# Kernel tuning notes

Hardware: AMD Instinct MI355X
Metric: run time of the kernel (lower is better)

The kernel has to match this reference:

```python
import jax, jax.numpy as jnp
import numpy as np
from jax import lax

B, C, N = 4, 512, 4096
NH = 8
HD = C // NH          # 64
SR = 2                # sr_ratio
EPS = 1e-5            # BatchNorm eps (torch default)


def setup_inputs() -> dict:
    key = jax.random.key(0)
    ks = jax.random.split(key, 12)
    d = {}
    d["x"] = jax.random.normal(ks[0], (B, C, N), jnp.float32)
    d["y"] = jax.random.normal(ks[1], (B, C, N), jnp.float32)  # unused by forward (faithful to source)
    # Conv1d kernel-size-1 weights == (out_c, in_c) matrices; trunc_normal std=0.02 ~ normal*0.02
    d["Wq"] = jax.random.normal(ks[2], (C, C), jnp.float32) * 0.02
    d["Wk"] = jax.random.normal(ks[3], (C, C), jnp.float32) * 0.02
    # sr: Conv2d(dim, dim, kernel=SR, stride=SR), kaiming-ish init per _init_weights
    fan_out = SR * SR * C
    d["Wsr"] = jax.random.normal(ks[4], (C, C, SR, SR), jnp.float32) * np.sqrt(2.0 / fan_out)
    d["bsr"] = jnp.zeros((C,), jnp.float32)
    # BatchNorm1d(dim) in inference mode
    d["bn_gamma"] = 1.0 + 0.1 * jax.random.normal(ks[5], (C,), jnp.float32)
    d["bn_beta"] = 0.1 * jax.random.normal(ks[6], (C,), jnp.float32)
    d["bn_mean"] = 0.1 * jax.random.normal(ks[7], (C,), jnp.float32)
    d["bn_var"] = 1.0 + 0.1 * jnp.abs(jax.random.normal(ks[8], (C,), jnp.float32))
    d["Wproj"] = jax.random.normal(ks[9], (C, C), jnp.float32) * 0.02
    d["bproj"] = jnp.zeros((C,), jnp.float32)
    d["H"] = 64
    d["W"] = 64
    return d


def reference(x, y, Wq, Wk, Wsr, bsr, bn_gamma, bn_beta, bn_mean, bn_var, Wproj, bproj, H, W):
    scale = HD ** -0.5
    # q: Conv1d(k=1) -> (B,C,N) -> (B,NH,HD,N) -> (B,NH,N,HD)
    q = jnp.einsum('oc,bcn->bon', Wq, x).reshape(B, NH, HD, N).transpose(0, 1, 3, 2)
    # spatial reduction path (sr_ratio > 1): Conv2d stride SR, then BN (inference), then k-proj
    x4 = x.reshape(B, C, H, W)
    xsr = lax.conv_general_dilated(x4, Wsr, (SR, SR), 'VALID',
                                   dimension_numbers=('NCHW', 'OIHW', 'NCHW'))
    xsr = xsr + bsr[None, :, None, None]
    xsr = xsr.reshape(B, C, -1)  # (B, C, Nk), Nk = (H//SR)*(W//SR)
    inv_std = lax.rsqrt(bn_var + EPS)
    xsr = (xsr - bn_mean[None, :, None]) * (inv_std * bn_gamma)[None, :, None] + bn_beta[None, :, None]
    k = jnp.einsum('oc,bcn->bon', Wk, xsr).reshape(B, NH, HD, -1)  # (B,NH,HD,Nk)
    # v: mean over tokens, replicated per head -> effectively (B, C)
    v = jnp.mean(x, axis=2)  # (B, C)
    # scores + max over keys (no softmax)
    attn = jnp.einsum('bhnd,bhdk->bhnk', q, k) * scale  # (B,NH,N,Nk)
    attn = jnp.max(attn, axis=-1)                        # (B,NH,N)
    # out[b,c,n] = sum_h attn[b,h,n] * v[b,c]  (attn^T @ v, then transpose)
    out = jnp.sum(attn, axis=1)[:, None, :] * v[:, :, None]  # (B,C,N)
    out = jnp.einsum('oc,bcn->bon', Wproj, out) + bproj[None, :, None]
    return out
```

## Files before the change

### kernel.cpp

```cpp
#include <hip/hip_runtime.h>
#include <hip/hip_bf16.h>

constexpr int B_ = 4, C_ = 512, N_ = 4096, NH_ = 8, HD_ = 64;
constexpr int NK = 1024;
constexpr float SCALE = 0.125f;
constexpr float EPS = 1e-5f;

typedef __attribute__((ext_vector_type(8))) short bf16x8;
typedef __attribute__((ext_vector_type(4))) float f32x4;

__device__ __forceinline__ short bf16s(float f) {
    __hip_bfloat16 h = __float2bfloat16(f);
    return *reinterpret_cast<short*>(&h);
}
__device__ __forceinline__ float bf2f(short s) {
    return __bfloat162float(*reinterpret_cast<__hip_bfloat16*>(&s));
}

#define GLD16(gp, lp)                                                                     \
    __builtin_amdgcn_global_load_lds((const __attribute__((address_space(1))) void*)(gp), \
                                     (__attribute__((address_space(3))) void*)(lp), 16, 0, 0)

__global__ __launch_bounds__(256) void k_xw(const float* __restrict__ x,
                                            const float* __restrict__ Wq, const float* __restrict__ Wk,
// ... 45 lines not shown
            Wkp16[o * C_ + c] = bf16s(wk * sc);
            Wq16[o * C_ + c] = bf16s(Wq[o * C_ + c]);
            acc += wk * (sc * (bsr[c] - mean[c]) + beta[c]);
        }
        for (int m = 32; m; m >>= 1) acc += __shfl_xor(acc, m);
        if ((tid & 63) == 0) t[0][tid >> 6] = acc;
        __syncthreads();
        if (tid == 0) bk[o] = t[0][0] + t[0][1] + t[0][2] + t[0][3];
    } else {
        const int r = bid - 2560, kt = r & 31, ot = r >> 5;
        {
            const int cc = tid >> 2, q = tid & 3;
            const float* xr = Wsr + (size_t)(ot * 64 + cc) * 2048 + kt * 64;
#pragma unroll
            for (int jj = 0; jj < 4; ++jj) {
                float4 f = *reinterpret_cast<const float4*>(&xr[q * 16 + jj * 4]);
                int n = q * 16 + jj * 4;
                t[n + 0][cc] = f.x; t[n + 1][cc] = f.y;
                t[n + 2][cc] = f.z; t[n + 3][cc] = f.w;
            }
        }
        __syncthreads();
        {
            const int n = tid >> 2, c0 = (tid & 3) * 16;
            bf16x8 u0, u1;
#pragma unroll
            for (int j = 0; j < 8; ++j) {
                u0[j] = bf16s(t[n][c0 + j]);
                u1[j] = bf16s(t[n][c0 + 8 + j]);
            }
            int gkk = kt * 64 + n;
            int row2 = (gkk & 3) * 512 + (gkk >> 2);
            short* dst = WsrT + (size_t)row2 * C_ + ot * 64 + c0;
            *reinterpret_cast<bf16x8*>(dst) = u0;
            *reinterpret_cast<bf16x8*>(dst + 8) = u1;
        }
    }
}

template <int MT>
__device__ __forceinline__ void gemm_core(const short* __restrict__ Ag,
                                          const short* __restrict__ Bg, int K,
                                          short* Abuf, short* Bbuf,
                                          f32x4 (&acc)[MT][4]) {
    const int tid = threadIdx.x;
    const int w = tid >> 6, l = tid & 63;
    const int lr = l & 15, lg = l >> 4;
    const int wm = w >> 1, wn = w & 1;
    const int srow = tid >> 3, scol = (tid & 7) * 8;
    char* AbufC = (char*)Abuf;
    char* BbufC = (char*)Bbuf;
    for (int kt = 0; kt < K; kt += 64) {
#pragma unroll
        for (int i = 0; i < MT; ++i)
            GLD16(Ag + (size_t)(i * 32 + srow) * K + kt + scol, AbufC + i * 4096 + tid * 16);
#pragma unroll
        for (int i = 0; i < 4; ++i)
            GLD16(Bg + (size_t)(i * 32 + srow) * K + kt + scol, BbufC + i * 4096 + tid * 16);
        __syncthreads();
        bf16x8 af[MT][2], bfv[4][2];
#pragma unroll
        for (int mt = 0; mt < MT; ++mt)
#pragma unroll
            for (int ks = 0; ks < 2; ++ks)
                af[mt][ks] = *reinterpret_cast<const bf16x8*>(
                    &Abuf[(wm * MT * 16 + mt * 16 + lr) * 64 + ks * 32 + lg * 8]);
#pragma unroll
        for (int nt = 0; nt < 4; ++nt)
#pragma unroll
            for (int ks = 0; ks < 2; ++ks)
                bfv[nt][ks] = *reinterpret_cast<const bf16x8*>(
                    &Bbuf[(wn * 64 + nt * 16 + lr) * 64 + ks * 32 + lg * 8]);
#pragma unroll
        for (int mt = 0; mt < MT; ++mt)
#pragma unroll
            for (int nt = 0; nt < 4; ++nt) {
                acc[mt][nt] = __builtin_amdgcn_mfma_f32_16x16x32_bf16(af[mt][0], bfv[nt][0], acc[mt][nt], 0, 0, 0);
                acc[mt][nt] = __builtin_amdgcn_mfma_f32_16x16x32_bf16(af[mt][1], bfv[nt][1], acc[mt][nt], 0, 0, 0);
            }
        __syncthreads();
    }
}

__global__ __launch_bounds__(256) void k_wck64(const short* __restrict__ WsrT,
                                               const short* __restrict__ Wkp16,
                                               short* __restrict__ Wck16) {
    __shared__ short Ab[64 * 64];
    __shared__ short Bb[64 * 64];
    const int m0 = blockIdx.x * 64;
    const int n0 = blockIdx.y * 64;
    const int tid = threadIdx.x, w = tid >> 6, l = tid & 63;
    const int lr = l & 15, lg = l >> 4, wm = w >> 1, wn = w & 1;
    const int srow = tid >> 3, scol = (tid & 7) * 8;
    f32x4 acc[2][2];
#pragma unroll
    for (int i = 0; i < 2; ++i)
#pragma unroll
        for (int j = 0; j < 2; ++j) acc[i][j] = (f32x4){0.f, 0.f, 0.f, 0.f};
    char* AbC = (char*)Ab;
    char* BbC = (char*)Bb;
    for (int kt = 0; kt < 512; kt += 64) {
#pragma unroll
        for (int j = 0; j < 2; ++j) {
            GLD16(WsrT + (size_t)(m0 + j * 32 + srow) * 512 + kt + scol, AbC + j * 4096 + tid * 16);
            GLD16(Wkp16 + (size_t)(n0 + j * 32 + srow) * 512 + kt + scol, BbC + j * 4096 + tid * 16);
        }
        __syncthreads();
        bf16x8 af[2][2], bfv[2][2];
#pragma unroll
        for (int mt = 0; mt < 2; ++mt)
#pragma unroll
            for (int ks = 0; ks < 2; ++ks)
                af[mt][ks] = *reinterpret_cast<const bf16x8*>(
                    &Ab[(wm * 32 + mt * 16 + lr) * 64 + ks * 32 + lg * 8]);
#pragma unroll
        for (int nt = 0; nt < 2; ++nt)
#pragma unroll
            for (int ks = 0; ks < 2; ++ks)
                bfv[nt][ks] = *reinterpret_cast<const bf16x8*>(
                    &Bb[(wn * 32 + nt * 16 + lr) * 64 + ks * 32 + lg * 8]);
#pragma unroll
        for (int mt = 0; mt < 2; ++mt)
#pragma unroll
            for (int nt = 0; nt < 2; ++nt) {
                acc[mt][nt] = __builtin_amdgcn_mfma_f32_16x16x32_bf16(af[mt][0], bfv[nt][0], acc[mt][nt], 0, 0, 0);
                acc[mt][nt] = __builtin_amdgcn_mfma_f32_16x16x32_bf16(af[mt][1], bfv[nt][1], acc[mt][nt], 0, 0, 0);
            }
        __syncthreads();
    }
#pragma unroll
    for (int mt = 0; mt < 2; ++mt)
#pragma unroll
        for (int nt = 0; nt < 2; ++nt) {
            int kk0 = m0 + wm * 32 + mt * 16 + lg * 4;
            int o = n0 + wn * 32 + nt * 16 + lr;
            short4 u;
            u.x = bf16s(acc[mt][nt][0]);
            u.y = bf16s(acc[mt][nt][1]);
            u.z = bf16s(acc[mt][nt][2]);
            u.w = bf16s(acc[mt][nt][3]);
            *reinterpret_cast<short4*>(&Wck16[(size_t)o * 2048 + kk0]) = u;
        }
}

__global__ __launch_bounds__(256) void k_gemm_qk2(const short* __restrict__ xT,
                                                  const short* __restrict__ Wq16,
                                                  const short* __restrict__ Wck16,
                                                  short* __restrict__ kp,
                                                  short* __restrict__ q2) {
    __shared__ short Abuf[128 * 64];
    __shared__ short Bbuf[128 * 64];
    f32x4 acc[4][4];
#pragma unroll
    for (int i = 0; i < 4; ++i)
#pragma unroll
        for (int j = 0; j < 4; ++j) acc[i][j] = (f32x4){0.f, 0.f, 0.f, 0.f};
    const int bid = blockIdx.x;
    const int tid = threadIdx.x, l = tid & 63, w = tid >> 6;
    const int lr = l & 15, lg = l >> 4, wm = w >> 1, wn = w & 1;
    const int srow = tid >> 3, scol = (tid & 7) * 8;
    char* AbufC = (char*)Abuf;
    char* BbufC = (char*)Bbuf;

    if (bid < 512) {
        const int s = bid >> 7;
        const int dy = s >> 1, dx = s & 1;
        const int r2 = bid & 127;
        const int n0 = (r2 >> 2) * 128;
        const int m0 = (r2 & 3) * 128;
        for (int kt2 = 0; kt2 < 512; kt2 += 64) {
#pragma unroll
            for (int i = 0; i < 4; ++i) {
                int bp = n0 + i * 32 + srow;
                int b = bp >> 10, p = bp & 1023;
                int n = ((p >> 5) * 2 + dy) * 64 + (p & 31) * 2 + dx;
                GLD16(xT + ((size_t)(b * N_ + n)) * C_ + kt2 + scol, AbufC + i * 4096 + tid * 16);
            }
#pragma unroll
            for (int i = 0; i < 4; ++i)
                GLD16(Wck16 + (size_t)(m0 + i * 32 + srow) * 2048 + s * 512 + kt2 + scol,
                      BbufC + i * 4096 + tid * 16);
            __syncthreads();
            bf16x8 af[4][2], bfv[4][2];
#pragma unroll
            for (int mt = 0; mt < 4; ++mt)
#pragma unroll
                for (int ks = 0; ks < 2; ++ks)
                    af[mt][ks] = *reinterpret_cast<const bf16x8*>(
                        &Abuf[(wm * 64 + mt * 16 + lr) * 64 + ks * 32 + lg * 8]);
#pragma unroll
            for (int nt = 0; nt < 4; ++nt)
#pragma unroll
                for (int ks = 0; ks < 2; ++ks)
                    bfv[nt][ks] = *reinterpret_cast<const bf16x8*>(
                        &Bbuf[(wn * 64 + nt * 16 + lr) * 64 + ks * 32 + lg * 8]);
#pragma unroll
            for (int mt = 0; mt < 4; ++mt)
#pragma unroll
                for (int nt = 0; nt < 4; ++nt) {
                    acc[mt][nt] = __builtin_amdgcn_mfma_f32_16x16x32_bf16(af[mt][0], bfv[nt][0], acc[mt][nt], 0, 0, 0);
                    acc[mt][nt] = __builtin_amdgcn_mfma_f32_16x16x32_bf16(af[mt][1], bfv[nt][1], acc[mt][nt], 0, 0, 0);
                }
            __syncthreads();
        }
        short* kps = kp + (size_t)s * (4096 * 512);
#pragma unroll
        for (int mt = 0; mt < 4; ++mt)
#pragma unroll
            for (int nt = 0; nt < 4; ++nt) {
                int o = m0 + wn * 64 + nt * 16 + lr;
#pragma unroll
                for (int r = 0; r < 4; ++r) {
                    int bp = n0 + wm * 64 + mt * 16 + lg * 4 + r;
                    kps[(size_t)bp * 512 + o] = bf16s(acc[mt][nt][r]);
                }
            }
    } else {
        const int bq = bid - 512;
        const int m0 = (bq & 3) * 128, n0 = (bq >> 2) * 128;
        gemm_core<4>(Wq16 + (size_t)m0 * 512, xT + (size_t)n0 * 512, 512, Abuf, Bbuf, acc);
#pragma unroll
        for (int mt = 0; mt < 4; ++mt) {
            const int o0 = m0 + wm * 64 + mt * 16 + lg * 4;
            const int h = o0 >> 6, d0 = o0 & 63;
#pragma unroll
            for (int nt = 0; nt < 4; ++nt) {
                int ng = n0 + wn * 64 + nt * 16 + lr;
                int b = ng >> 12, n = ng & 4095;
                short4 u;
                u.x = bf16s(acc[mt][nt][0]);
                u.y = bf16s(acc[mt][nt][1]);
                u.z = bf16s(acc[mt][nt][2]);
                u.w = bf16s(acc[mt][nt][3]);
                *reinterpret_cast<short4*>(&q2[(((size_t)(b * NH_ + h)) * N_ + n) * HD_ + d0]) = u;
            }
        }
    }
}

__global__ __launch_bounds__(256) void k_kredpv(const short* __restrict__ kp,
                                                const float* __restrict__ bk,
                                                const float* __restrict__ vpart,
                                                const float* __restrict__ Wproj,
                                                short* __restrict__ k3,
                                                float* __restrict__ pv) {
    const int bid = blockIdx.x, tid = threadIdx.x;
    if (bid < 4096) {
        const int bp = bid, b = bp >> 10, p = bp & 1023;
        const int o = tid * 2;
        const short* k0 = kp + (size_t)bp * 512 + o;
        float2 bb = *reinterpret_cast<const float2*>(&bk[o]);
        float sx = bb.x, sy = bb.y;
#pragma unroll
        for (int s = 0; s < 4; ++s) {
            short2 v2 = *reinterpret_cast<const short2*>(k0 + (size_t)s * (4096 * 512));
            sx += bf2f(v2.x);
            sy += bf2f(v2.y);
        }
        short2 u;
        u.x = bf16s(sx);
        u.y = bf16s(sy);
        const int h = o >> 6, d = o & 63;
        *reinterpret_cast<short2*>(&k3[(((size_t)(b * NH_ + h)) * NK + p) * HD_ + d]) = u;
    } else {
        const int r = bid - 4096, oc = r & 7, b = r >> 3;
        __shared__ float vs[512];
        float2 s = {0.f, 0.f};
        for (int y = 0; y < 64; ++y) {
            float2 f = *reinterpret_cast<const float2*>(&vpart[((size_t)(y * B_ + b)) * C_ + tid * 2]);
            s.x += f.x; s.y += f.y;
        }
        vs[tid * 2] = s.x * (1.f / N_);
        vs[tid * 2 + 1] = s.y * (1.f / N_);
        __syncthreads();
        const int w = tid >> 6, l = tid & 63;
#pragma unroll 4
        for (int i = 0; i < 16; ++i) {
            int o = oc * 64 + i * 4 + w;
            const float* wr = Wproj + (size_t)o * C_;
            float4 a = *reinterpret_cast<const float4*>(&wr[l * 8]);
            float4 b4 = *reinterpret_cast<const float4*>(&wr[l * 8 + 4]);
            float acc = a.x * vs[l * 8] + a.y * vs[l * 8 + 1] + a.z * vs[l * 8 + 2] + a.w * vs[l * 8 + 3] +
                        b4.x * vs[l * 8 + 4] + b4.y * vs[l * 8 + 5] + b4.z * vs[l * 8 + 6] + b4.w * vs[l * 8 + 7];
            for (int m = 32; m; m >>= 1) acc += __shfl_xor(acc, m);
            if (l == 0) pv[b * C_ + o] = acc;
        }
    }
}

__global__ __launch_bounds__(256) void k_attn3(const short* __restrict__ k3,
                                               const short* __restrict__ q2,
                                               float* __restrict__ am) {
    const int b = blockIdx.z, h = blockIdx.y, n0 = blockIdx.x * 256;
    const int w = threadIdx.x >> 6, l = threadIdx.x & 63;
    const int lr = l & 15, lg = l >> 4;
    const short* qb = q2 + ((size_t)(b * NH_ + h)) * N_ * HD_;
    const short* kb = k3 + ((size_t)(b * NH_ + h)) * NK * HD_;

    bf16x8 bq[16][2];
#pragma unroll
    for (int nt = 0; nt < 16; ++nt)
#pragma unroll
        for (int ks = 0; ks < 2; ++ks)
            bq[nt][ks] = *reinterpret_cast<const bf16x8*>(
                &qb[(size_t)(n0 + nt * 16 + lr) * HD_ + ks * 32 + lg * 8]);

    float rmax[16];
#pragma unroll
    for (int nt = 0; nt < 16; ++nt) rmax[nt] = -3.4e38f;

    const short* kw = kb + (size_t)(w * 256) * HD_;
    const short* s0 = kw + (size_t)lr * HD_ + lg * 8;
    bf16x8 a0 = *reinterpret_cast<const bf16x8*>(s0);
    bf16x8 a1 = *reinterpret_cast<const bf16x8*>(s0 + 32);
    for (int t = 0; t < 16; ++t) {
        bf16x8 c0 = a0, c1 = a1;
        if (t < 15) {
            const short* s2 = kw + (size_t)((t + 1) * 16 + lr) * HD_ + lg * 8;
            a0 = *reinterpret_cast<const bf16x8*>(s2);
            a1 = *reinterpret_cast<const bf16x8*>(s2 + 32);
        }
        __builtin_amdgcn_s_setprio(1);
#pragma unroll
        for (int nt = 0; nt < 16; ++nt) {
            f32x4 acc = {0.f, 0.f, 0.f, 0.f};
            acc = __builtin_amdgcn_mfma_f32_16x16x32_bf16(c0, bq[nt][0], acc, 0, 0, 0);
            acc = __builtin_amdgcn_mfma_f32_16x16x32_bf16(c1, bq[nt][1], acc, 0, 0, 0);
            rmax[nt] = fmaxf(fmaxf(fmaxf(fmaxf(acc[0], acc[1]), acc[2]), acc[3]), rmax[nt]);
        }
        __builtin_amdgcn_s_setprio(0);
    }
#pragma unroll
    for (int nt = 0; nt < 16; ++nt) {
        float m = rmax[nt];
        m = fmaxf(m, __shfl_xor(m, 16));
        m = fmaxf(m, __shfl_xor(m, 32));
        rmax[nt] = m;
    }
    __shared__ float sm[4][256];
    if (lg == 0) {
#pragma unroll
        for (int nt = 0; nt < 16; ++nt) sm[w][nt * 16 + lr] = rmax[nt];
    }
    __syncthreads();
    {
        const int tid = threadIdx.x;
        float m = fmaxf(fmaxf(sm[0][tid], sm[1][tid]),
                        fmaxf(sm[2][tid], sm[3][tid]));
        am[((size_t)(b * NH_ + h)) * N_ + n0 + tid] = SCALE * m;
    }
}

__global__ __launch_bounds__(256) void k_final(const float* __restrict__ pv, const float* __restrict__ am,
                                               const float* __restrict__ bproj, float* __restrict__ out) {
    const int b = blockIdx.z, o0 = blockIdx.y * 64 + (threadIdx.x >> 5) * 8;
    const int n = blockIdx.x * 128 + (threadIdx.x & 31) * 4;
    float4 s = {0.f, 0.f, 0.f, 0.f};
#pragma unroll
    for (int h = 0; h < NH_; ++h) {
        float4 a = *reinterpret_cast<const float4*>(&am[((size_t)(b * NH_ + h)) * N_ + n]);
        s.x += a.x; s.y += a.y; s.z += a.z; s.w += a.w;
    }
    float* ob = out + (size_t)b * C_ * N_ + n;
    const float* pvb = pv + b * C_;
#pragma unroll
    for (int i = 0; i < 8; ++i) {
        int o = o0 + i;
        float p = pvb[o], bp = bproj[o];
        float4 r = {p * s.x + bp, p * s.y + bp, p * s.z + bp, p * s.w + bp};
        *reinterpret_cast<float4*>(&ob[(size_t)o * N_]) = r;
    }
}

extern "C" void kernel_launch(void* const* d_in, const int* in_sizes, int n_in,
                              void* d_out, int out_size, void* d_ws, size_t ws_size,
                              hipStream_t stream) {
    const float* x     = (const float*)d_in[0];
    const float* Wq    = (const float*)d_in[2];
    const float* Wk    = (const float*)d_in[3];
    const float* Wsr   = (const float*)d_in[4];
    const float* bsr   = (const float*)d_in[5];
    const float* gamma = (const float*)d_in[6];
    const float* beta  = (const float*)d_in[7];
    const float* mean  = (const float*)d_in[8];
    const float* var   = (const float*)d_in[9];
    const float* Wproj = (const float*)d_in[10];
    const float* bproj = (const float*)d_in[11];
    float* out = (float*)d_out;

    char* ws = (char*)d_ws;
    float* vpart = (float*)(ws + 0);
    float* pv    = (float*)(ws + 524288);
    float* bk    = (float*)(ws + 532480);
    float* am    = (float*)(ws + 536576);
    short* Wq16  = (short*)(ws + 1060864);
    short* Wkp16 = (short*)(ws + 1585152);
    short* WsrT  = (short*)(ws + 2109440);
    short* Wck16 = (short*)(ws + 4206592);
    short* xT    = (short*)(ws + 6303744);
    short* q2    = (short*)(ws + 23080960);
    short* k3    = (short*)(ws + 39858176);
    short* kp    = (short*)(ws + 44052480);

    k_xw<<<dim3(2816), 256, 0, stream>>>(x, Wq, Wk, gamma, beta, mean, var, bsr, Wsr,
                                         xT, vpart, Wq16, Wkp16, bk, WsrT);
    k_wck64<<<dim3(32, 8), 256, 0, stream>>>(WsrT, Wkp16, Wck16);
    k_gemm_qk2<<<dim3(1024), 256, 0, stream>>>(xT, Wq16, Wck16, kp, q2);
    k_kredpv<<<dim3(4128), 256, 0, stream>>>(kp, bk, vpart, Wproj, k3, pv);
    k_attn3<<<dim3(16, NH_, B_), 256, 0, stream>>>(k3, q2, am);
    k_final<<<dim3(32, 8, B_), 256, 0, stream>>>(pv, am, bproj, out);
}
```

Baseline: 101.8 us.

## Fuse attention max with output projection and merge pv into weight-combine kernel

```diff
diff --git a/kernel.cpp b/kernel.cpp
--- a/kernel.cpp
+++ b/kernel.cpp
@@ -151,188 +151,72 @@
     }
 }
 
-__global__ __launch_bounds__(256) void k_wck64(const short* __restrict__ WsrT,
+__global__ __launch_bounds__(256) void k_wckpv(const short* __restrict__ WsrT,
                                                const short* __restrict__ Wkp16,
-                                               short* __restrict__ Wck16) {
-    __shared__ short Ab[64 * 64];
-    __shared__ short Bb[64 * 64];
-    const int m0 = blockIdx.x * 64;
-    const int n0 = blockIdx.y * 64;
-    const int tid = threadIdx.x, w = tid >> 6, l = tid & 63;
-    const int lr = l & 15, lg = l >> 4, wm = w >> 1, wn = w & 1;
-    const int srow = tid >> 3, scol = (tid & 7) * 8;
-    f32x4 acc[2][2];
-#pragma unroll
-    for (int i = 0; i < 2; ++i)
-#pragma unroll
-        for (int j = 0; j < 2; ++j) acc[i][j] = (f32x4){0.f, 0.f, 0.f, 0.f};
-    char* AbC = (char*)Ab;
-    char* BbC = (char*)Bb;
-    for (int kt = 0; kt < 512; kt += 64) {
-#pragma unroll
-        for (int j = 0; j < 2; ++j) {
-            GLD16(WsrT + (size_t)(m0 + j * 32 + srow) * 512 + kt + scol, AbC + j * 4096 + tid * 16);
-            GLD16(Wkp16 + (size_t)(n0 + j * 32 + srow) * 512 + kt + scol, BbC + j * 4096 + tid * 16);
-        }
-        __syncthreads();
-        bf16x8 af[2][2], bfv[2][2];
-#pragma unroll
-        for (int mt = 0; mt < 2; ++mt)
-#pragma unroll
-            for (int ks = 0; ks < 2; ++ks)
-                af[mt][ks] = *reinterpret_cast<const bf16x8*>(
-                    &Ab[(wm * 32 + mt * 16 + lr) * 64 + ks * 32 + lg * 8]);
-#pragma unroll
-        for (int nt = 0; nt < 2; ++nt)
-#pragma unroll
-            for (int ks = 0; ks < 2; ++ks)
-                bfv[nt][ks] = *reinterpret_cast<const bf16x8*>(
-                    &Bb[(wn * 32 + nt * 16 + lr) * 64 + ks * 32 + lg * 8]);
-#pragma unroll
-        for (int mt = 0; mt < 2; ++mt)
-#pragma unroll
-            for (int nt = 0; nt < 2; ++nt) {
-                acc[mt][nt] = __builtin_amdgcn_mfma_f32_16x16x32_bf16(af[mt][0], bfv[nt][0], acc[mt][nt], 0, 0, 0);
-                acc[mt][nt] = __builtin_amdgcn_mfma_f32_16x16x32_bf16(af[mt][1], bfv[nt][1], acc[mt][nt], 0, 0, 0);
-            }
-        __syncthreads();
-    }
-#pragma unroll
-    for (int mt = 0; mt < 2; ++mt)
-#pragma unroll
-        for (int nt = 0; nt < 2; ++nt) {
-            int kk0 = m0 + wm * 32 + mt * 16 + lg * 4;
-            int o = n0 + wn * 32 + nt * 16 + lr;
-            short4 u;
-            u.x = bf16s(acc[mt][nt][0]);
-            u.y = bf16s(acc[mt][nt][1]);
-            u.z = bf16s(acc[mt][nt][2]);
-            u.w = bf16s(acc[mt][nt][3]);
-            *reinterpret_cast<short4*>(&Wck16[(size_t)o * 2048 + kk0]) = u;
-        }
-}
-
-__global__ __launch_bounds__(256) void k_gemm_qk2(const short* __restrict__ xT,
-                                                  const short* __restrict__ Wq16,
-                                                  const short* __restrict__ Wck16,
-                                                  short* __restrict__ kp,
-                                                  short* __restrict__ q2) {
-    __shared__ short Abuf[128 * 64];
-    __shared__ short Bbuf[128 * 64];
-    f32x4 acc[4][4];
-#pragma unroll
-    for (int i = 0; i < 4; ++i)
-#pragma unroll
-        for (int j = 0; j < 4; ++j) acc[i][j] = (f32x4){0.f, 0.f, 0.f, 0.f};
-    const int bid = blockIdx.x;
-    const int tid = threadIdx.x, l = tid & 63, w = tid >> 6;
-    const int lr = l & 15, lg = l >> 4, wm = w >> 1, wn = w & 1;
-    const int srow = tid >> 3, scol = (tid & 7) * 8;
-    char* AbufC = (char*)Abuf;
-    char* BbufC = (char*)Bbuf;
-
-    if (bid < 512) {
-        const int s = bid >> 7;
-        const int dy = s >> 1, dx = s & 1;
-        const int r2 = bid & 127;
-        const int n0 = (r2 >> 2) * 128;
-        const int m0 = (r2 & 3) * 128;
-        for (int kt2 = 0; kt2 < 512; kt2 += 64) {
-#pragma unroll
-            for (int i = 0; i < 4; ++i) {
-                int bp = n0 + i * 32 + srow;
-                int b = bp >> 10, p = bp & 1023;
-                int n = ((p >> 5) * 2 + dy) * 64 + (p & 31) * 2 + dx;
-                GLD16(xT + ((size_t)(b * N_ + n)) * C_ + kt2 + scol, AbufC + i * 4096 + tid * 16);
-            }
-#pragma unroll
-            for (int i = 0; i < 4; ++i)
-                GLD16(Wck16 + (size_t)(m0 + i * 32 + srow) * 2048 + s * 512 + kt2 + scol,
-                      BbufC + i * 4096 + tid * 16);
+                                               const float* __restrict__ vpart,
+                                               const float* __restrict__ Wproj,
+                                               short* __restrict__ Wck16,
+                                               float* __restrict__ pv) {
+    const int bid = blockIdx.x, tid = threadIdx.x;
+    if (bid < 256) {
+        __shared__ short Ab[64 * 64];
+        __shared__ short Bb[64 * 64];
+        const int m0 = (bid & 31) * 64;
+        const int n0 = (bid >> 5) * 64;
+        const int w = tid >> 6, l = tid & 63;
+        const int lr = l & 15, lg = l >> 4, wm = w >> 1, wn = w & 1;
+        const int srow = tid >> 3, scol = (tid & 7) * 8;
+        f32x4 acc[2][2];
+#pragma unroll
+        for (int i = 0; i < 2; ++i)
+#pragma unroll
+            for (int j = 0; j < 2; ++j) acc[i][j] = (f32x4){0.f, 0.f, 0.f, 0.f};
+        char* AbC = (char*)Ab;
+        char* BbC = (char*)Bb;
+        for (int kt = 0; kt < 512; kt += 64) {
+#pragma unroll
+            for (int j = 0; j < 2; ++j) {
+                GLD16(WsrT + (size_t)(m0 + j * 32 + srow) * 512 + kt + scol, AbC + j * 4096 + tid * 16);
+                GLD16(Wkp16 + (size_t)(n0 + j * 32 + srow) * 512 + kt + scol, BbC + j * 4096 + tid * 16);
+            }
             __syncthreads();
-            bf16x8 af[4][2], bfv[4][2];
-#pragma unroll
-            for (int mt = 0; mt < 4; ++mt)
+            bf16x8 af[2][2], bfv[2][2];
+#pragma unroll
+            for (int mt = 0; mt < 2; ++mt)
 #pragma unroll
                 for (int ks = 0; ks < 2; ++ks)
                     af[mt][ks] = *reinterpret_cast<const bf16x8*>(
-                        &Abuf[(wm * 64 + mt * 16 + lr) * 64 + ks * 32 + lg * 8]);
-#pragma unroll
-            for (int nt = 0; nt < 4; ++nt)
+                        &Ab[(wm * 32 + mt * 16 + lr) * 64 + ks * 32 + lg * 8]);
+#pragma unroll
+            for (int nt = 0; nt < 2; ++nt)
 #pragma unroll
                 for (int ks = 0; ks < 2; ++ks)
                     bfv[nt][ks] = *reinterpret_cast<const bf16x8*>(
-                        &Bbuf[(wn * 64 + nt * 16 + lr) * 64 + ks * 32 + lg * 8]);
-#pragma unroll
-            for (int mt = 0; mt < 4; ++mt)
-#pragma unroll
-                for (int nt = 0; nt < 4; ++nt) {
+                        &Bb[(wn * 32 + nt * 16 + lr) * 64 + ks * 32 + lg * 8]);
+#pragma unroll
+            for (int mt = 0; mt < 2; ++mt)
+#pragma unroll
+                for (int nt = 0; nt < 2; ++nt) {
                     acc[mt][nt] = __builtin_amdgcn_mfma_f32_16x16x32_bf16(af[mt][0], bfv[nt][0], acc[mt][nt], 0, 0, 0);
                     acc[mt][nt] = __builtin_amdgcn_mfma_f32_16x16x32_bf16(af[mt][1], bfv[nt][1], acc[mt][nt], 0, 0, 0);
                 }
             __syncthreads();
         }
-        short* kps = kp + (size_t)s * (4096 * 512);
-#pragma unroll
-        for (int mt = 0; mt < 4; ++mt)
-#pragma unroll
-            for (int nt = 0; nt < 4; ++nt) {
-                int o = m0 + wn * 64 + nt * 16 + lr;
-#pragma unroll
-                for (int r = 0; r < 4; ++r) {
-                    int bp = n0 + wm * 64 + mt * 16 + lg * 4 + r;
-                    kps[(size_t)bp * 512 + o] = bf16s(acc[mt][nt][r]);
-                }
-            }
-    } else {
-        const int bq = bid - 512;
-        const int m0 = (bq & 3) * 128, n0 = (bq >> 2) * 128;
-        gemm_core<4>(Wq16 + (size_t)m0 * 512, xT + (size_t)n0 * 512, 512, Abuf, Bbuf, acc);
-#pragma unroll
-        for (int mt = 0; mt < 4; ++mt) {
-            const int o0 = m0 + wm * 64 + mt * 16 + lg * 4;
-            const int h = o0 >> 6, d0 = o0 & 63;
-#pragma unroll
-            for (int nt = 0; nt < 4; ++nt) {
-                int ng = n0 + wn * 64 + nt * 16 + lr;
-                int b = ng >> 12, n = ng & 4095;
+#pragma unroll
+        for (int mt = 0; mt < 2; ++mt)
+#pragma unroll
+            for (int nt = 0; nt < 2; ++nt) {
+                int kk0 = m0 + wm * 32 + mt * 16 + lg * 4;
+                int o = n0 + wn * 32 + nt * 16 + lr;
                 short4 u;
                 u.x = bf16s(acc[mt][nt][0]);
                 u.y = bf16s(acc[mt][nt][1]);
                 u.z = bf16s(acc[mt][nt][2]);
                 u.w = bf16s(acc[mt][nt][3]);
-                *reinterpret_cast<short4*>(&q2[(((size_t)(b * NH_ + h)) * N_ + n) * HD_ + d0]) = u;
-            }
-        }
-    }
-}
-
-__global__ __launch_bounds__(256) void k_kredpv(const short* __restrict__ kp,
-                                                const float* __restrict__ bk,
-                                                const float* __restrict__ vpart,
-                                                const float* __restrict__ Wproj,
-                                                short* __restrict__ k3,
-                                                float* __restrict__ pv) {
-    const int bid = blockIdx.x, tid = threadIdx.x;
-    if (bid < 4096) {
-        const int bp = bid, b = bp >> 10, p = bp & 1023;
-        const int o = tid * 2;
-        const short* k0 = kp + (size_t)bp * 512 + o;
-        float2 bb = *reinterpret_cast<const float2*>(&bk[o]);
-        float sx = bb.x, sy = bb.y;
-#pragma unroll
-        for (int s = 0; s < 4; ++s) {
-            short2 v2 = *reinterpret_cast<const short2*>(k0 + (size_t)s * (4096 * 512));
-            sx += bf2f(v2.x);
-            sy += bf2f(v2.y);
-        }
-        short2 u;
-        u.x = bf16s(sx);
-        u.y = bf16s(sy);
-        const int h = o >> 6, d = o & 63;
-        *reinterpret_cast<short2*>(&k3[(((size_t)(b * NH_ + h)) * NK + p) * HD_ + d]) = u;
+                *reinterpret_cast<short4*>(&Wck16[(size_t)o * 2048 + kk0]) = u;
+            }
     } else {
-        const int r = bid - 4096, oc = r & 7, b = r >> 3;
+        const int r = bid - 256, oc = r & 7, b = r >> 3;
         __shared__ float vs[512];
         float2 s = {0.f, 0.f};
         for (int y = 0; y < 64; ++y) {
@@ -357,87 +241,201 @@
     }
 }
 
-__global__ __launch_bounds__(256) void k_attn3(const short* __restrict__ k3,
+__global__ __launch_bounds__(256) void k_gemm_qk2(const short* __restrict__ xT,
+                                                  const short* __restrict__ Wq16,
+                                                  const short* __restrict__ Wck16,
+                                                  short* __restrict__ kp,
+                                                  short* __restrict__ q2) {
+    __shared__ short Abuf[128 * 64];
+    __shared__ short Bbuf[128 * 64];
+    f32x4 acc[4][4];
+#pragma unroll
+    for (int i = 0; i < 4; ++i)
+#pragma unroll
+        for (int j = 0; j < 4; ++j) acc[i][j] = (f32x4){0.f, 0.f, 0.f, 0.f};
+    const int bid = (blockIdx.x & 7) * 128 + (blockIdx.x >> 3);
+    const int tid = threadIdx.x, l = tid & 63, w = tid >> 6;
+    const int lr = l & 15, lg = l >> 4, wm = w >> 1, wn = w & 1;
+    const int srow = tid >> 3, scol = (tid & 7) * 8;
+    char* AbufC = (char*)Abuf;
+    char* BbufC = (char*)Bbuf;
+
+    if (bid < 512) {
+        const int s = bid >> 7;
+        const int dy = s >> 1, dx = s & 1;
+        const int r2 = bid & 127;
+        const int n0 = (r2 >> 2) * 128;
+        const int m0 = (r2 & 3) * 128;
+        for (int kt2 = 0; kt2 < 512; kt2 += 64) {
+#pragma unroll
+            for (int i = 0; i < 4; ++i) {
+                int bp = n0 + i * 32 + srow;
+                int b = bp >> 10, p = bp & 1023;
+                int n = ((p >> 5) * 2 + dy) * 64 + (p & 31) * 2 + dx;
+                GLD16(xT + ((size_t)(b * N_ + n)) * C_ + kt2 + scol, AbufC + i * 4096 + tid * 16);
+            }
+#pragma unroll
+            for (int i = 0; i < 4; ++i)
+                GLD16(Wck16 + (size_t)(m0 + i * 32 + srow) * 2048 + s * 512 + kt2 + scol,
+                      BbufC + i * 4096 + tid * 16);
+            __syncthreads();
+            bf16x8 af[4][2], bfv[4][2];
+#pragma unroll
+            for (int mt = 0; mt < 4; ++mt)
+#pragma unroll
+                for (int ks = 0; ks < 2; ++ks)
+                    af[mt][ks] = *reinterpret_cast<const bf16x8*>(
+                        &Abuf[(wm * 64 + mt * 16 + lr) * 64 + ks * 32 + lg * 8]);
+#pragma unroll
+            for (int nt = 0; nt < 4; ++nt)
+#pragma unroll
+                for (int ks = 0; ks < 2; ++ks)
+                    bfv[nt][ks] = *reinterpret_cast<const bf16x8*>(
+                        &Bbuf[(wn * 64 + nt * 16 + lr) * 64 + ks * 32 + lg * 8]);
+#pragma unroll
+            for (int mt = 0; mt < 4; ++mt)
+#pragma unroll
+                for (int nt = 0; nt < 4; ++nt) {
+                    acc[mt][nt] = __builtin_amdgcn_mfma_f32_16x16x32_bf16(af[mt][0], bfv[nt][0], acc[mt][nt], 0, 0, 0);
+                    acc[mt][nt] = __builtin_amdgcn_mfma_f32_16x16x32_bf16(af[mt][1], bfv[nt][1], acc[mt][nt], 0, 0, 0);
+                }
+            __syncthreads();
+        }
+        short* kps = kp + (size_t)s * (4096 * 512);
+#pragma unroll
+        for (int mt = 0; mt < 4; ++mt)
+#pragma unroll
+            for (int nt = 0; nt < 4; ++nt) {
+                int o = m0 + wn * 64 + nt * 16 + lr;
+#pragma unroll
+                for (int r = 0; r < 4; ++r) {
+                    int bp = n0 + wm * 64 + mt * 16 + lg * 4 + r;
+                    kps[(size_t)bp * 512 + o] = bf16s(acc[mt][nt][r]);
+                }
+            }
+    } else {
+        const int bq = bid - 512;
+        const int m0 = (bq & 3) * 128, n0 = (bq >> 2) * 128;
+        gemm_core<4>(Wq16 + (size_t)m0 * 512, xT + (size_t)n0 * 512, 512, Abuf, Bbuf, acc);
+#pragma unroll
+        for (int mt = 0; mt < 4; ++mt) {
+            const int o0 = m0 + wm * 64 + mt * 16 + lg * 4;
+            const int h = o0 >> 6, d0 = o0 & 63;
+#pragma unroll
+            for (int nt = 0; nt < 4; ++nt) {
+                int ng = n0 + wn * 64 + nt * 16 + lr;
+                int b = ng >> 12, n = ng & 4095;
+                short4 u;
+                u.x = bf16s(acc[mt][nt][0]);
+                u.y = bf16s(acc[mt][nt][1]);
+                u.z = bf16s(acc[mt][nt][2]);
+                u.w = bf16s(acc[mt][nt][3]);
+                *reinterpret_cast<short4*>(&q2[(((size_t)(b * NH_ + h)) * N_ + n) * HD_ + d0]) = u;
+            }
+        }
+    }
+}
+
+__global__ __launch_bounds__(256) void k_kred(const short* __restrict__ kp,
+                                              const float* __restrict__ bk,
+                                              short* __restrict__ k3) {
+    const int r = blockIdx.x * 4 + (threadIdx.x >> 6);
+    const int o0 = (threadIdx.x & 63) * 8;
+    const int b = r >> 10, p = r & 1023;
+    const short* base = kp + (size_t)r * 512 + o0;
+    float s[8];
+    float4 b0 = *reinterpret_cast<const float4*>(&bk[o0]);
+    float4 b1 = *reinterpret_cast<const float4*>(&bk[o0 + 4]);
+    s[0] = b0.x; s[1] = b0.y; s[2] = b0.z; s[3] = b0.w;
+    s[4] = b1.x; s[5] = b1.y; s[6] = b1.z; s[7] = b1.w;
+#pragma unroll
+    for (int sp = 0; sp < 4; ++sp) {
+        bf16x8 v = *reinterpret_cast<const bf16x8*>(base + (size_t)sp * (4096 * 512));
+#pragma unroll
+        for (int j = 0; j < 8; ++j) s[j] += bf2f(v[j]);
+    }
+    bf16x8 u;
+#pragma unroll
+    for (int j = 0; j < 8; ++j) u[j] = bf16s(s[j]);
+    const int h = o0 >> 6, d = o0 & 63;
+    *reinterpret_cast<bf16x8*>(&k3[(((size_t)(b * NH_ + h)) * NK + p) * HD_ + d]) = u;
+}
+
+__global__ __launch_bounds__(512) void k_attnf(const short* __restrict__ k3,
                                                const short* __restrict__ q2,
-                                               float* __restrict__ am) {
-    const int b = blockIdx.z, h = blockIdx.y, n0 = blockIdx.x * 256;
-    const int w = threadIdx.x >> 6, l = threadIdx.x & 63;
+                                               const float* __restrict__ pv,
+                                               const float* __restrict__ bproj,
+                                               float* __restrict__ out) {
+    const int b = blockIdx.y, n0 = blockIdx.x * 64;
+    const int tid = threadIdx.x, w = tid >> 6, l = tid & 63;
     const int lr = l & 15, lg = l >> 4;
-    const short* qb = q2 + ((size_t)(b * NH_ + h)) * N_ * HD_;
-    const short* kb = k3 + ((size_t)(b * NH_ + h)) * NK * HD_;
-
-    bf16x8 bq[16][2];
-#pragma unroll
-    for (int nt = 0; nt < 16; ++nt)
-#pragma unroll
-        for (int ks = 0; ks < 2; ++ks)
-            bq[nt][ks] = *reinterpret_cast<const bf16x8*>(
-                &qb[(size_t)(n0 + nt * 16 + lr) * HD_ + ks * 32 + lg * 8]);
-
-    float rmax[16];
-#pragma unroll
-    for (int nt = 0; nt < 16; ++nt) rmax[nt] = -3.4e38f;
-
-    const short* kw = kb + (size_t)(w * 256) * HD_;
-    const short* s0 = kw + (size_t)lr * HD_ + lg * 8;
-    bf16x8 a0 = *reinterpret_cast<const bf16x8*>(s0);
-    bf16x8 a1 = *reinterpret_cast<const bf16x8*>(s0 + 32);
-    for (int t = 0; t < 16; ++t) {
-        bf16x8 c0 = a0, c1 = a1;
-        if (t < 15) {
-            const short* s2 = kw + (size_t)((t + 1) * 16 + lr) * HD_ + lg * 8;
-            a0 = *reinterpret_cast<const bf16x8*>(s2);
-            a1 = *reinterpret_cast<const bf16x8*>(s2 + 32);
-        }
-        __builtin_amdgcn_s_setprio(1);
-#pragma unroll
-        for (int nt = 0; nt < 16; ++nt) {
-            f32x4 acc = {0.f, 0.f, 0.f, 0.f};
-            acc = __builtin_amdgcn_mfma_f32_16x16x32_bf16(c0, bq[nt][0], acc, 0, 0, 0);
-            acc = __builtin_amdgcn_mfma_f32_16x16x32_bf16(c1, bq[nt][1], acc, 0, 0, 0);
-            rmax[nt] = fmaxf(fmaxf(fmaxf(fmaxf(acc[0], acc[1]), acc[2]), acc[3]), rmax[nt]);
-        }
-        __builtin_amdgcn_s_setprio(0);
-    }
-#pragma unroll
-    for (int nt = 0; nt < 16; ++nt) {
-        float m = rmax[nt];
-        m = fmaxf(m, __shfl_xor(m, 16));
-        m = fmaxf(m, __shfl_xor(m, 32));
-        rmax[nt] = m;
-    }
-    __shared__ float sm[4][256];
-    if (lg == 0) {
-#pragma unroll
-        for (int nt = 0; nt < 16; ++nt) sm[w][nt * 16 + lr] = rmax[nt];
-    }
-    __syncthreads();
-    {
-        const int tid = threadIdx.x;
-        float m = fmaxf(fmaxf(sm[0][tid], sm[1][tid]),
-                        fmaxf(sm[2][tid], sm[3][tid]));
-        am[((size_t)(b * NH_ + h)) * N_ + n0 + tid] = SCALE * m;
-    }
-}
-
-__global__ __launch_bounds__(256) void k_final(const float* __restrict__ pv, const float* __restrict__ am,
-                                               const float* __restrict__ bproj, float* __restrict__ out) {
-    const int b = blockIdx.z, o0 = blockIdx.y * 64 + (threadIdx.x >> 5) * 8;
-    const int n = blockIdx.x * 128 + (threadIdx.x & 31) * 4;
-    float4 s = {0.f, 0.f, 0.f, 0.f};
-#pragma unroll
+    __shared__ float sm[8][64];
+    __shared__ float ssum[64];
+    if (tid < 64) ssum[tid] = 0.f;
+
     for (int h = 0; h < NH_; ++h) {
-        float4 a = *reinterpret_cast<const float4*>(&am[((size_t)(b * NH_ + h)) * N_ + n]);
-        s.x += a.x; s.y += a.y; s.z += a.z; s.w += a.w;
-    }
-    float* ob = out + (size_t)b * C_ * N_ + n;
+        const short* qb = q2 + ((size_t)(b * NH_ + h)) * N_ * HD_;
+        const short* kb = k3 + ((size_t)(b * NH_ + h)) * NK * HD_ + (size_t)(w * 128) * HD_;
+        bf16x8 bq[4][2];
+#pragma unroll
+        for (int nt = 0; nt < 4; ++nt)
+#pragma unroll
+            for (int ks = 0; ks < 2; ++ks)
+                bq[nt][ks] = *reinterpret_cast<const bf16x8*>(
+                    &qb[(size_t)(n0 + nt * 16 + lr) * HD_ + ks * 32 + lg * 8]);
+        float rmax[4];
+#pragma unroll
+        for (int nt = 0; nt < 4; ++nt) rmax[nt] = -3.4e38f;
+
+        const short* s0p = kb + (size_t)lr * HD_ + lg * 8;
+        bf16x8 a0 = *reinterpret_cast<const bf16x8*>(s0p);
+        bf16x8 a1 = *reinterpret_cast<const bf16x8*>(s0p + 32);
+        for (int t = 0; t < 8; ++t) {
+            bf16x8 c0 = a0, c1 = a1;
+            if (t < 7) {
+                const short* s2 = kb + (size_t)((t + 1) * 16 + lr) * HD_ + lg * 8;
+                a0 = *reinterpret_cast<const bf16x8*>(s2);
+                a1 = *reinterpret_cast<const bf16x8*>(s2 + 32);
+            }
+            __builtin_amdgcn_s_setprio(1);
+#pragma unroll
+            for (int nt = 0; nt < 4; ++nt) {
+                f32x4 acc = {0.f, 0.f, 0.f, 0.f};
+                acc = __builtin_amdgcn_mfma_f32_16x16x32_bf16(c0, bq[nt][0], acc, 0, 0, 0);
+                acc = __builtin_amdgcn_mfma_f32_16x16x32_bf16(c1, bq[nt][1], acc, 0, 0, 0);
+                rmax[nt] = fmaxf(fmaxf(fmaxf(fmaxf(acc[0], acc[1]), acc[2]), acc[3]), rmax[nt]);
+            }
+            __builtin_amdgcn_s_setprio(0);
+        }
+#pragma unroll
+        for (int nt = 0; nt < 4; ++nt) {
+            float m = rmax[nt];
+            m = fmaxf(m, __shfl_xor(m, 16));
+            m = fmaxf(m, __shfl_xor(m, 32));
+            rmax[nt] = m;
+        }
+        if (lg == 0) {
+#pragma unroll
+            for (int nt = 0; nt < 4; ++nt) sm[w][nt * 16 + lr] = rmax[nt];
+        }
+        __syncthreads();
+        if (tid < 64) {
+            float m = sm[0][tid];
+#pragma unroll
+            for (int ww = 1; ww < 8; ++ww) m = fmaxf(m, sm[ww][tid]);
+            ssum[tid] += SCALE * m;
+        }
+        __syncthreads();
+    }
     const float* pvb = pv + b * C_;
-#pragma unroll
-    for (int i = 0; i < 8; ++i) {
-        int o = o0 + i;
+    float* ob = out + (size_t)b * C_ * N_ + n0;
+    float4 sv = *reinterpret_cast<const float4*>(&ssum[(tid & 15) * 4]);
+#pragma unroll 4
+    for (int pass = 0; pass < 16; ++pass) {
+        int o = pass * 32 + (tid >> 4);
         float p = pvb[o], bp = bproj[o];
-        float4 r = {p * s.x + bp, p * s.y + bp, p * s.z + bp, p * s.w + bp};
-        *reinterpret_cast<float4*>(&ob[(size_t)o * N_]) = r;
+        float4 rr = {p * sv.x + bp, p * sv.y + bp, p * sv.z + bp, p * sv.w + bp};
+        *reinterpret_cast<float4*>(&ob[(size_t)o * N_ + (tid & 15) * 4]) = rr;
     }
 }
 
@@ -461,7 +459,6 @@
     float* vpart = (float*)(ws + 0);
     float* pv    = (float*)(ws + 524288);
     float* bk    = (float*)(ws + 532480);
-    float* am    = (float*)(ws + 536576);
     short* Wq16  = (short*)(ws + 1060864);
     short* Wkp16 = (short*)(ws + 1585152);
     short* WsrT  = (short*)(ws + 2109440);
@@ -473,9 +470,8 @@
 
     k_xw<<<dim3(2816), 256, 0, stream>>>(x, Wq, Wk, gamma, beta, mean, var, bsr, Wsr,
                                          xT, vpart, Wq16, Wkp16, bk, WsrT);
-    k_wck64<<<dim3(32, 8), 256, 0, stream>>>(WsrT, Wkp16, Wck16);
+    k_wckpv<<<dim3(288), 256, 0, stream>>>(WsrT, Wkp16, vpart, Wproj, Wck16, pv);
     k_gemm_qk2<<<dim3(1024), 256, 0, stream>>>(xT, Wq16, Wck16, kp, q2);
-    k_kredpv<<<dim3(4128), 256, 0, stream>>>(kp, bk, vpart, Wproj, k3, pv);
-    k_attn3<<<dim3(16, NH_, B_), 256, 0, stream>>>(k3, q2, am);
-    k_final<<<dim3(32, 8, B_), 256, 0, stream>>>(pv, am, bproj, out);
-}
+    k_kred<<<dim3(1024), 256, 0, stream>>>(kp, bk, k3);
+    k_attnf<<<dim3(64, B_), 512, 0, stream>>>(k3, q2, pv, bproj, out);
+}
```

Measured after the change: 123.2 us. 1.21x slower.

## Move pv projection into weight-combine kernel, vectorize k reduction, swizzle GEMM blocks

Applied to the files above, without the earlier changes.

```diff
diff --git a/kernel.cpp b/kernel.cpp
--- a/kernel.cpp
+++ b/kernel.cpp
@@ -151,188 +151,72 @@
     }
 }
 
-__global__ __launch_bounds__(256) void k_wck64(const short* __restrict__ WsrT,
+__global__ __launch_bounds__(256) void k_wckpv(const short* __restrict__ WsrT,
                                                const short* __restrict__ Wkp16,
-                                               short* __restrict__ Wck16) {
-    __shared__ short Ab[64 * 64];
-    __shared__ short Bb[64 * 64];
-    const int m0 = blockIdx.x * 64;
-    const int n0 = blockIdx.y * 64;
-    const int tid = threadIdx.x, w = tid >> 6, l = tid & 63;
-    const int lr = l & 15, lg = l >> 4, wm = w >> 1, wn = w & 1;
-    const int srow = tid >> 3, scol = (tid & 7) * 8;
-    f32x4 acc[2][2];
-#pragma unroll
-    for (int i = 0; i < 2; ++i)
-#pragma unroll
-        for (int j = 0; j < 2; ++j) acc[i][j] = (f32x4){0.f, 0.f, 0.f, 0.f};
-    char* AbC = (char*)Ab;
-    char* BbC = (char*)Bb;
-    for (int kt = 0; kt < 512; kt += 64) {
-#pragma unroll
-        for (int j = 0; j < 2; ++j) {
-            GLD16(WsrT + (size_t)(m0 + j * 32 + srow) * 512 + kt + scol, AbC + j * 4096 + tid * 16);
-            GLD16(Wkp16 + (size_t)(n0 + j * 32 + srow) * 512 + kt + scol, BbC + j * 4096 + tid * 16);
-        }
-        __syncthreads();
-        bf16x8 af[2][2], bfv[2][2];
-#pragma unroll
-        for (int mt = 0; mt < 2; ++mt)
-#pragma unroll
-            for (int ks = 0; ks < 2; ++ks)
-                af[mt][ks] = *reinterpret_cast<const bf16x8*>(
-                    &Ab[(wm * 32 + mt * 16 + lr) * 64 + ks * 32 + lg * 8]);
-#pragma unroll
-        for (int nt = 0; nt < 2; ++nt)
-#pragma unroll
-            for (int ks = 0; ks < 2; ++ks)
-                bfv[nt][ks] = *reinterpret_cast<const bf16x8*>(
-                    &Bb[(wn * 32 + nt * 16 + lr) * 64 + ks * 32 + lg * 8]);
-#pragma unroll
-        for (int mt = 0; mt < 2; ++mt)
-#pragma unroll
-            for (int nt = 0; nt < 2; ++nt) {
-                acc[mt][nt] = __builtin_amdgcn_mfma_f32_16x16x32_bf16(af[mt][0], bfv[nt][0], acc[mt][nt], 0, 0, 0);
-                acc[mt][nt] = __builtin_amdgcn_mfma_f32_16x16x32_bf16(af[mt][1], bfv[nt][1], acc[mt][nt], 0, 0, 0);
-            }
-        __syncthreads();
-    }
-#pragma unroll
-    for (int mt = 0; mt < 2; ++mt)
-#pragma unroll
-        for (int nt = 0; nt < 2; ++nt) {
-            int kk0 = m0 + wm * 32 + mt * 16 + lg * 4;
-            int o = n0 + wn * 32 + nt * 16 + lr;
-            short4 u;
-            u.x = bf16s(acc[mt][nt][0]);
-            u.y = bf16s(acc[mt][nt][1]);
-            u.z = bf16s(acc[mt][nt][2]);
-            u.w = bf16s(acc[mt][nt][3]);
-            *reinterpret_cast<short4*>(&Wck16[(size_t)o * 2048 + kk0]) = u;
-        }
-}
-
-__global__ __launch_bounds__(256) void k_gemm_qk2(const short* __restrict__ xT,
-                                                  const short* __restrict__ Wq16,
-                                                  const short* __restrict__ Wck16,
-                                                  short* __restrict__ kp,
-                                                  short* __restrict__ q2) {
-    __shared__ short Abuf[128 * 64];
-    __shared__ short Bbuf[128 * 64];
-    f32x4 acc[4][4];
-#pragma unroll
-    for (int i = 0; i < 4; ++i)
-#pragma unroll
-        for (int j = 0; j < 4; ++j) acc[i][j] = (f32x4){0.f, 0.f, 0.f, 0.f};
-    const int bid = blockIdx.x;
-    const int tid = threadIdx.x, l = tid & 63, w = tid >> 6;
-    const int lr = l & 15, lg = l >> 4, wm = w >> 1, wn = w & 1;
-    const int srow = tid >> 3, scol = (tid & 7) * 8;
-    char* AbufC = (char*)Abuf;
-    char* BbufC = (char*)Bbuf;
-
-    if (bid < 512) {
-        const int s = bid >> 7;
-        const int dy = s >> 1, dx = s & 1;
-        const int r2 = bid & 127;
-        const int n0 = (r2 >> 2) * 128;
-        const int m0 = (r2 & 3) * 128;
-        for (int kt2 = 0; kt2 < 512; kt2 += 64) {
-#pragma unroll
-            for (int i = 0; i < 4; ++i) {
-                int bp = n0 + i * 32 + srow;
-                int b = bp >> 10, p = bp & 1023;
-                int n = ((p >> 5) * 2 + dy) * 64 + (p & 31) * 2 + dx;
-                GLD16(xT + ((size_t)(b * N_ + n)) * C_ + kt2 + scol, AbufC + i * 4096 + tid * 16);
-            }
-#pragma unroll
-            for (int i = 0; i < 4; ++i)
-                GLD16(Wck16 + (size_t)(m0 + i * 32 + srow) * 2048 + s * 512 + kt2 + scol,
-                      BbufC + i * 4096 + tid * 16);
+                                               const float* __restrict__ vpart,
+                                               const float* __restrict__ Wproj,
+                                               short* __restrict__ Wck16,
+                                               float* __restrict__ pv) {
+    const int bid = blockIdx.x, tid = threadIdx.x;
+    if (bid < 256) {
+        __shared__ short Ab[64 * 64];
+        __shared__ short Bb[64 * 64];
+        const int m0 = (bid & 31) * 64;
+        const int n0 = (bid >> 5) * 64;
+        const int w = tid >> 6, l = tid & 63;
+        const int lr = l & 15, lg = l >> 4, wm = w >> 1, wn = w & 1;
+        const int srow = tid >> 3, scol = (tid & 7) * 8;
+        f32x4 acc[2][2];
+#pragma unroll
+        for (int i = 0; i < 2; ++i)
+#pragma unroll
+            for (int j = 0; j < 2; ++j) acc[i][j] = (f32x4){0.f, 0.f, 0.f, 0.f};
+        char* AbC = (char*)Ab;
+        char* BbC = (char*)Bb;
+        for (int kt = 0; kt < 512; kt += 64) {
+#pragma unroll
+            for (int j = 0; j < 2; ++j) {
+                GLD16(WsrT + (size_t)(m0 + j * 32 + srow) * 512 + kt + scol, AbC + j * 4096 + tid * 16);
+                GLD16(Wkp16 + (size_t)(n0 + j * 32 + srow) * 512 + kt + scol, BbC + j * 4096 + tid * 16);
+            }
             __syncthreads();
-            bf16x8 af[4][2], bfv[4][2];
-#pragma unroll
-            for (int mt = 0; mt < 4; ++mt)
+            bf16x8 af[2][2], bfv[2][2];
+#pragma unroll
+            for (int mt = 0; mt < 2; ++mt)
 #pragma unroll
                 for (int ks = 0; ks < 2; ++ks)
                     af[mt][ks] = *reinterpret_cast<const bf16x8*>(
-                        &Abuf[(wm * 64 + mt * 16 + lr) * 64 + ks * 32 + lg * 8]);
-#pragma unroll
-            for (int nt = 0; nt < 4; ++nt)
+                        &Ab[(wm * 32 + mt * 16 + lr) * 64 + ks * 32 + lg * 8]);
+#pragma unroll
+            for (int nt = 0; nt < 2; ++nt)
 #pragma unroll
                 for (int ks = 0; ks < 2; ++ks)
                     bfv[nt][ks] = *reinterpret_cast<const bf16x8*>(
-                        &Bbuf[(wn * 64 + nt * 16 + lr) * 64 + ks * 32 + lg * 8]);
-#pragma unroll
-            for (int mt = 0; mt < 4; ++mt)
-#pragma unroll
-                for (int nt = 0; nt < 4; ++nt) {
+                        &Bb[(wn * 32 + nt * 16 + lr) * 64 + ks * 32 + lg * 8]);
+#pragma unroll
+            for (int mt = 0; mt < 2; ++mt)
+#pragma unroll
+                for (int nt = 0; nt < 2; ++nt) {
                     acc[mt][nt] = __builtin_amdgcn_mfma_f32_16x16x32_bf16(af[mt][0], bfv[nt][0], acc[mt][nt], 0, 0, 0);
                     acc[mt][nt] = __builtin_amdgcn_mfma_f32_16x16x32_bf16(af[mt][1], bfv[nt][1], acc[mt][nt], 0, 0, 0);
                 }
             __syncthreads();
         }
-        short* kps = kp + (size_t)s * (4096 * 512);
-#pragma unroll
-        for (int mt = 0; mt < 4; ++mt)
-#pragma unroll
-            for (int nt = 0; nt < 4; ++nt) {
-                int o = m0 + wn * 64 + nt * 16 + lr;
-#pragma unroll
-                for (int r = 0; r < 4; ++r) {
-                    int bp = n0 + wm * 64 + mt * 16 + lg * 4 + r;
-                    kps[(size_t)bp * 512 + o] = bf16s(acc[mt][nt][r]);
-                }
-            }
-    } else {
-        const int bq = bid - 512;
-        const int m0 = (bq & 3) * 128, n0 = (bq >> 2) * 128;
-        gemm_core<4>(Wq16 + (size_t)m0 * 512, xT + (size_t)n0 * 512, 512, Abuf, Bbuf, acc);
-#pragma unroll
-        for (int mt = 0; mt < 4; ++mt) {
-            const int o0 = m0 + wm * 64 + mt * 16 + lg * 4;
-            const int h = o0 >> 6, d0 = o0 & 63;
-#pragma unroll
-            for (int nt = 0; nt < 4; ++nt) {
-                int ng = n0 + wn * 64 + nt * 16 + lr;
-                int b = ng >> 12, n = ng & 4095;
+#pragma unroll
+        for (int mt = 0; mt < 2; ++mt)
+#pragma unroll
+            for (int nt = 0; nt < 2; ++nt) {
+                int kk0 = m0 + wm * 32 + mt * 16 + lg * 4;
+                int o = n0 + wn * 32 + nt * 16 + lr;
                 short4 u;
                 u.x = bf16s(acc[mt][nt][0]);
                 u.y = bf16s(acc[mt][nt][1]);
                 u.z = bf16s(acc[mt][nt][2]);
                 u.w = bf16s(acc[mt][nt][3]);
-                *reinterpret_cast<short4*>(&q2[(((size_t)(b * NH_ + h)) * N_ + n) * HD_ + d0]) = u;
-            }
-        }
-    }
-}
-
-__global__ __launch_bounds__(256) void k_kredpv(const short* __restrict__ kp,
-                                                const float* __restrict__ bk,
-                                                const float* __restrict__ vpart,
-                                                const float* __restrict__ Wproj,
-                                                short* __restrict__ k3,
-                                                float* __restrict__ pv) {
-    const int bid = blockIdx.x, tid = threadIdx.x;
-    if (bid < 4096) {
-        const int bp = bid, b = bp >> 10, p = bp & 1023;
-        const int o = tid * 2;
-        const short* k0 = kp + (size_t)bp * 512 + o;
-        float2 bb = *reinterpret_cast<const float2*>(&bk[o]);
-        float sx = bb.x, sy = bb.y;
-#pragma unroll
-        for (int s = 0; s < 4; ++s) {
-            short2 v2 = *reinterpret_cast<const short2*>(k0 + (size_t)s * (4096 * 512));
-            sx += bf2f(v2.x);
-            sy += bf2f(v2.y);
-        }
-        short2 u;
-        u.x = bf16s(sx);
-        u.y = bf16s(sy);
-        const int h = o >> 6, d = o & 63;
-        *reinterpret_cast<short2*>(&k3[(((size_t)(b * NH_ + h)) * NK + p) * HD_ + d]) = u;
+                *reinterpret_cast<short4*>(&Wck16[(size_t)o * 2048 + kk0]) = u;
+            }
     } else {
-        const int r = bid - 4096, oc = r & 7, b = r >> 3;
+        const int r = bid - 256, oc = r & 7, b = r >> 3;
         __shared__ float vs[512];
         float2 s = {0.f, 0.f};
         for (int y = 0; y < 64; ++y) {
@@ -355,6 +239,126 @@
             if (l == 0) pv[b * C_ + o] = acc;
         }
     }
+}
+
+__global__ __launch_bounds__(256) void k_gemm_qk2(const short* __restrict__ xT,
+                                                  const short* __restrict__ Wq16,
+                                                  const short* __restrict__ Wck16,
+                                                  short* __restrict__ kp,
+                                                  short* __restrict__ q2) {
+    __shared__ short Abuf[128 * 64];
+    __shared__ short Bbuf[128 * 64];
+    f32x4 acc[4][4];
+#pragma unroll
+    for (int i = 0; i < 4; ++i)
+#pragma unroll
+        for (int j = 0; j < 4; ++j) acc[i][j] = (f32x4){0.f, 0.f, 0.f, 0.f};
+    const int bid = (blockIdx.x & 7) * 128 + (blockIdx.x >> 3);
+    const int tid = threadIdx.x, l = tid & 63, w = tid >> 6;
+    const int lr = l & 15, lg = l >> 4, wm = w >> 1, wn = w & 1;
+    const int srow = tid >> 3, scol = (tid & 7) * 8;
+    char* AbufC = (char*)Abuf;
+    char* BbufC = (char*)Bbuf;
+
+    if (bid < 512) {
+        const int s = bid >> 7;
+        const int dy = s >> 1, dx = s & 1;
+        const int r2 = bid & 127;
+        const int n0 = (r2 >> 2) * 128;
+        const int m0 = (r2 & 3) * 128;
+        for (int kt2 = 0; kt2 < 512; kt2 += 64) {
+#pragma unroll
+            for (int i = 0; i < 4; ++i) {
+                int bp = n0 + i * 32 + srow;
+                int b = bp >> 10, p = bp & 1023;
+                int n = ((p >> 5) * 2 + dy) * 64 + (p & 31) * 2 + dx;
+                GLD16(xT + ((size_t)(b * N_ + n)) * C_ + kt2 + scol, AbufC + i * 4096 + tid * 16);
+            }
+#pragma unroll
+            for (int i = 0; i < 4; ++i)
+                GLD16(Wck16 + (size_t)(m0 + i * 32 + srow) * 2048 + s * 512 + kt2 + scol,
+                      BbufC + i * 4096 + tid * 16);
+            __syncthreads();
+            bf16x8 af[4][2], bfv[4][2];
+#pragma unroll
+            for (int mt = 0; mt < 4; ++mt)
+#pragma unroll
+                for (int ks = 0; ks < 2; ++ks)
+                    af[mt][ks] = *reinterpret_cast<const bf16x8*>(
+                        &Abuf[(wm * 64 + mt * 16 + lr) * 64 + ks * 32 + lg * 8]);
+#pragma unroll
+            for (int nt = 0; nt < 4; ++nt)
+#pragma unroll
+                for (int ks = 0; ks < 2; ++ks)
+                    bfv[nt][ks] = *reinterpret_cast<const bf16x8*>(
+                        &Bbuf[(wn * 64 + nt * 16 + lr) * 64 + ks * 32 + lg * 8]);
+#pragma unroll
+            for (int mt = 0; mt < 4; ++mt)
+#pragma unroll
+                for (int nt = 0; nt < 4; ++nt) {
+                    acc[mt][nt] = __builtin_amdgcn_mfma_f32_16x16x32_bf16(af[mt][0], bfv[nt][0], acc[mt][nt], 0, 0, 0);
+                    acc[mt][nt] = __builtin_amdgcn_mfma_f32_16x16x32_bf16(af[mt][1], bfv[nt][1], acc[mt][nt], 0, 0, 0);
+                }
+            __syncthreads();
+        }
+        short* kps = kp + (size_t)s * (4096 * 512);
+#pragma unroll
+        for (int mt = 0; mt < 4; ++mt)
+#pragma unroll
+            for (int nt = 0; nt < 4; ++nt) {
+                int o = m0 + wn * 64 + nt * 16 + lr;
+#pragma unroll
+                for (int r = 0; r < 4; ++r) {
+                    int bp = n0 + wm * 64 + mt * 16 + lg * 4 + r;
+                    kps[(size_t)bp * 512 + o] = bf16s(acc[mt][nt][r]);
+                }
+            }
+    } else {
+        const int bq = bid - 512;
+        const int m0 = (bq & 3) * 128, n0 = (bq >> 2) * 128;
+        gemm_core<4>(Wq16 + (size_t)m0 * 512, xT + (size_t)n0 * 512, 512, Abuf, Bbuf, acc);
+#pragma unroll
+        for (int mt = 0; mt < 4; ++mt) {
+            const int o0 = m0 + wm * 64 + mt * 16 + lg * 4;
+            const int h = o0 >> 6, d0 = o0 & 63;
+#pragma unroll
+            for (int nt = 0; nt < 4; ++nt) {
+                int ng = n0 + wn * 64 + nt * 16 + lr;
+                int b = ng >> 12, n = ng & 4095;
+                short4 u;
+                u.x = bf16s(acc[mt][nt][0]);
+                u.y = bf16s(acc[mt][nt][1]);
+                u.z = bf16s(acc[mt][nt][2]);
+                u.w = bf16s(acc[mt][nt][3]);
+                *reinterpret_cast<short4*>(&q2[(((size_t)(b * NH_ + h)) * N_ + n) * HD_ + d0]) = u;
+            }
+        }
+    }
+}
+
+__global__ __launch_bounds__(256) void k_kred(const short* __restrict__ kp,
+                                              const float* __restrict__ bk,
+                                              short* __restrict__ k3) {
+    const int r = blockIdx.x * 4 + (threadIdx.x >> 6);
+    const int o0 = (threadIdx.x & 63) * 8;
+    const int b = r >> 10, p = r & 1023;
+    const short* base = kp + (size_t)r * 512 + o0;
+    float s[8];
+    float4 b0 = *reinterpret_cast<const float4*>(&bk[o0]);
+    float4 b1 = *reinterpret_cast<const float4*>(&bk[o0 + 4]);
+    s[0] = b0.x; s[1] = b0.y; s[2] = b0.z; s[3] = b0.w;
+    s[4] = b1.x; s[5] = b1.y; s[6] = b1.z; s[7] = b1.w;
+#pragma unroll
+    for (int sp = 0; sp < 4; ++sp) {
+        bf16x8 v = *reinterpret_cast<const bf16x8*>(base + (size_t)sp * (4096 * 512));
+#pragma unroll
+        for (int j = 0; j < 8; ++j) s[j] += bf2f(v[j]);
+    }
+    bf16x8 u;
+#pragma unroll
+    for (int j = 0; j < 8; ++j) u[j] = bf16s(s[j]);
+    const int h = o0 >> 6, d = o0 & 63;
+    *reinterpret_cast<bf16x8*>(&k3[(((size_t)(b * NH_ + h)) * NK + p) * HD_ + d]) = u;
 }
 
 __global__ __launch_bounds__(256) void k_attn3(const short* __restrict__ k3,
@@ -473,9 +477,9 @@
 
     k_xw<<<dim3(2816), 256, 0, stream>>>(x, Wq, Wk, gamma, beta, mean, var, bsr, Wsr,
                                          xT, vpart, Wq16, Wkp16, bk, WsrT);
-    k_wck64<<<dim3(32, 8), 256, 0, stream>>>(WsrT, Wkp16, Wck16);
+    k_wckpv<<<dim3(288), 256, 0, stream>>>(WsrT, Wkp16, vpart, Wproj, Wck16, pv);
     k_gemm_qk2<<<dim3(1024), 256, 0, stream>>>(xT, Wq16, Wck16, kp, q2);
-    k_kredpv<<<dim3(4128), 256, 0, stream>>>(kp, bk, vpart, Wproj, k3, pv);
+    k_kred<<<dim3(1024), 256, 0, stream>>>(kp, bk, k3);
     k_attn3<<<dim3(16, NH_, B_), 256, 0, stream>>>(k3, q2, am);
     k_final<<<dim3(32, 8, B_), 256, 0, stream>>>(pv, am, bproj, out);
 }
```

New measurement: 92.26 us (median of 3 runs). -9.4%, faster.
